# Optimization experiments

Hardware: AMD Instinct MI355X
Metric: run time of the kernel (lower is better)

## Reference

```python
import jax, jax.numpy as jnp
import numpy as np

B, S, E = 2, 2048, 2048
H, KV, D = 32, 8, 128
EPS = 1e-6


def _rope_tables(seq_len, head_dim, base=1_000_000.0):
    inv_freq = 1.0 / (base ** (np.arange(0, head_dim, 2, dtype=np.float32) / head_dim))
    ang = np.arange(seq_len, dtype=np.float32)[:, None] * inv_freq[None, :]  # [S, D/2]
    cos = np.concatenate([np.cos(ang), np.cos(ang)], axis=-1)  # [S, D]
    sin = np.concatenate([np.sin(ang), np.sin(ang)], axis=-1)
    return jnp.asarray(cos), jnp.asarray(sin)


def setup_inputs() -> dict:
    key = jax.random.key(0)
    ks = jax.random.split(key, 8)
    x = jax.random.normal(ks[0], (B, S, E), dtype=jnp.float32)
    mask = jnp.triu(jnp.ones((S, S), dtype=bool), k=1)  # True = masked (causal)
    cos, sin = _rope_tables(S, D)
    w = 0.02
    Wq = jax.random.normal(ks[1], (E, H * D), dtype=jnp.float32) * w
    bq = jnp.zeros((H * D,), dtype=jnp.float32)
    Wk = jax.random.normal(ks[2], (E, KV * D), dtype=jnp.float32) * w
    bk = jnp.zeros((KV * D,), dtype=jnp.float32)
    Wv = jax.random.normal(ks[3], (E, KV * D), dtype=jnp.float32) * w
    bv = jnp.zeros((KV * D,), dtype=jnp.float32)
    Wo = jax.random.normal(ks[4], (H * D, E), dtype=jnp.float32) * w
    q_scale = jnp.ones((D,), dtype=jnp.float32)
    k_scale = jnp.ones((D,), dtype=jnp.float32)
    return {"x": x, "mask": mask, "cos": cos, "sin": sin, "Wq": Wq, "bq": bq,
            "Wk": Wk, "bk": bk, "Wv": Wv, "bv": bv, "Wo": Wo,
            "q_scale": q_scale, "k_scale": k_scale}


def _rmsnorm(x, scale):
    xf = x.astype(jnp.float32)
    var = jnp.mean(xf * xf, axis=-1, keepdims=True)
    return (xf * jax.lax.rsqrt(var + EPS) * scale).astype(x.dtype)


def _apply_rope(x, cos, sin):
    # x: [B, h, S, D]; cos/sin: [S, D]
    d2 = x.shape[-1] // 2
    x1, x2 = x[..., :d2], x[..., d2:]
    rotated = jnp.concatenate([-x2, x1], axis=-1)
    return (x * cos[None, None] + rotated * sin[None, None]).astype(x.dtype)


def reference(x, mask, cos, sin, Wq, bq, Wk, bk, Wv, bv, Wo, q_scale, k_scale):
    b, s, _ = x.shape
    q = (x @ Wq + bq).reshape(b, s, H, D).transpose(0, 2, 1, 3)   # [B,H,S,D]
    k = (x @ Wk + bk).reshape(b, s, KV, D).transpose(0, 2, 1, 3)  # [B,KV,S,D]
    v = (x @ Wv + bv).reshape(b, s, KV, D).transpose(0, 2, 1, 3)
    q = _rmsnorm(q, q_scale)
    k = _rmsnorm(k, k_scale)
    q = _apply_rope(q, cos, sin)
    k = _apply_rope(k, cos, sin)
    group = H // KV
    k = jnp.repeat(k, group, axis=1)  # repeat_interleave on head dim -> [B,H,S,D]
    v = jnp.repeat(v, group, axis=1)
    scores = jnp.einsum("bhqd,bhkd->bhqk", q, k)
    scores = jnp.where(mask[None, None], -jnp.inf, scores)
    attn = jax.nn.softmax(scores / jnp.sqrt(jnp.float32(D)), axis=-1)
    ctx = jnp.einsum("bhqk,bhkd->bhqd", attn, v)
    ctx = ctx.transpose(0, 2, 1, 3).reshape(b, s, H * D)
    return ctx @ Wo
```

## Files before the change

### kernel.cpp

```cpp
#include <hip/hip_runtime.h>

typedef short short8 __attribute__((ext_vector_type(8)));
typedef float f32x4 __attribute__((ext_vector_type(4)));
typedef float f32x16 __attribute__((ext_vector_type(16)));
typedef unsigned int uint2v __attribute__((ext_vector_type(2)));

static __device__ __forceinline__ ushort f2bf(float f){
  union { float f; uint u; } cv; cv.f = f;
  uint u = cv.u;
  uint r = (u + 0x7fffu + ((u >> 16) & 1u)) >> 16;
  return (ushort)r;
}
static __device__ __forceinline__ float bf2f(ushort h){
  union { uint u; float f; } cv; cv.u = ((uint)h) << 16; return cv.f;
}
static __device__ __forceinline__ f32x4 mfma16x16x32(short8 a, short8 b, f32x4 c){
  return __builtin_amdgcn_mfma_f32_16x16x32_bf16(a, b, c, 0, 0, 0);
}
static __device__ __forceinline__ f32x16 mfma32(short8 a, short8 b, f32x16 c){
  return __builtin_amdgcn_mfma_f32_32x32x16_bf16(a, b, c, 0, 0, 0);
}
static __device__ __forceinline__ float ex2(float x){
  float r; asm("v_exp_f32 %0, %1" : "=v"(r) : "v"(x)); return r;
}
static __device__ __forceinline__ uint cvtpk(float lo, float hi){
  uint r; asm("v_cvt_pk_bf16_f32 %0, %1, %2" : "=v"(r) : "v"(lo), "v"(hi)); return r;
}
static __device__ __forceinline__ void glds16(const void* g, const void* l){
  __builtin_amdgcn_global_load_lds((const __attribute__((address_space(1))) void*)g,
                                   (__attribute__((address_space(3))) void*)l, 16, 0, 0);
}
static __device__ __forceinline__ void store_out(float* p, float v){ *p = v; }
static __device__ __forceinline__ void store_out(ushort* p, float v){ *p = f2bf(v); }
static __device__ __forceinline__ int xcd_swizzle(int flat, int nwg){
  int q = nwg >> 3, r = nwg & 7;
  int xcd = flat & 7, idx = flat >> 3;
  return (xcd < r) ? xcd * (q + 1) + idx : r * (q + 1) + (xcd - r) * q + idx;
}

__global__ void cvt_bf16_kernel(const float* __restrict__ x, ushort* __restrict__ y, int n4){
  int i = blockIdx.x * 256 + threadIdx.x;
  if (i < n4){
    float4 v = reinterpret_cast<const float4*>(x)[i];
    ushort4 o; o.x = f2bf(v.x); o.y = f2bf(v.y); o.z = f2bf(v.z); o.w = f2bf(v.w);
    reinterpret_cast<ushort4*>(y)[i] = o;
  }
}

__global__ void transpose_cvt_kernel(const float* __restrict__ W, ushort* __restrict__ WT, int K, int N){
  __shared__ float tile[32][33];
  int n0 = blockIdx.x * 32, k0 = blockIdx.y * 32;
  int tx = threadIdx.x, ty = threadIdx.y;
  #pragma unroll
  for (int i = 0; i < 4; i++){ int r = ty + i * 8; tile[r][tx] = W[(size_t)(k0 + r) * N + n0 + tx]; }
  __syncthreads();
  #pragma unroll
  for (int i = 0; i < 4; i++){ int r = ty + i * 8; WT[(size_t)(n0 + r) * K + k0 + tx] = f2bf(tile[tx][r]); }
}

__global__ void bias_concat_kernel(const float* __restrict__ bq, const float* __restrict__ bk,
                                   const float* __restrict__ bv, float* __restrict__ out){
  int i = blockIdx.x * 256 + threadIdx.x;
  if (i < 6144) out[i] = (i < 4096) ? bq[i] : ((i < 5120) ? bk[i - 4096] : bv[i - 5120]);
}

template<typename OutT>
__global__ __launch_bounds__(512, 2) void gemm256_kernel(const ushort* __restrict__ A, const ushort* __restrict__ BT,
                                                         const float* __restrict__ bias, OutT* __restrict__ C,
                                                         int M, int N, int K){
  __shared__ __align__(16) ushort As[2][128 * 64];
  __shared__ __align__(16) ushort Bs[2][256 * 64];
  const int nbx = N >> 8;
  const int nwg = nbx * (M >> 7);
  const int wg = xcd_swizzle(blockIdx.x, nwg);
  const int m0 = (wg / nbx) * 128, n0 = (wg % nbx) * 256;
  const int tid = threadIdx.x, w = tid >> 6, l = tid & 63, lm = l & 15, lk = l >> 4;
  const int wr = w >> 2, wc = w & 3;
  const int sr = tid >> 3, sc = tid & 7;
  const int scs = sc ^ (sr & 7);
  const int swz = lm & 7;
  const int nt = K >> 6;

#define STAGE_G(T, BUF) do{                                                                \
    _Pragma("unroll")                                                                      \
    for (int r = 0; r < 2; r++)                                                            \
      glds16(A + (size_t)(m0 + r * 64 + sr) * K + (size_t)(T) * 64 + scs * 8,              \
             &As[BUF][r * 4096 + w * 512]);                                                \
    _Pragma("unroll")                                                                      \
    for (int r = 0; r < 4; r++)                                                            \
      glds16(BT + (size_t)(n0 + r * 64 + sr) * K + (size_t)(T) * 64 + scs * 8,             \
             &Bs[BUF][r * 4096 + w * 512]);                                                \
  }while(0)

  f32x4 acc[4][4] = {};
  STAGE_G(0, 0);
  STAGE_G(1, 1);
  for (int t = 0; t < nt; t++){
    const int cur = t & 1;
    if (t < nt - 1) asm volatile("s_waitcnt vmcnt(6)" ::: "memory");
    else            asm volatile("s_waitcnt vmcnt(0)" ::: "memory");
    __builtin_amdgcn_s_barrier();
    asm volatile("" ::: "memory");
    short8 af[4][2], bf[4][2];
    #pragma unroll
    for (int mi = 0; mi < 4; mi++)
      #pragma unroll
      for (int ks = 0; ks < 2; ks++)
        af[mi][ks] = *(const short8*)&As[cur][(wr * 64 + mi * 16 + lm) * 64 + (((ks * 4 + lk) ^ swz) * 8)];
    #pragma unroll
    for (int ni = 0; ni < 4; ni++)
      #pragma unroll
      for (int ks = 0; ks < 2; ks++)
        bf[ni][ks] = *(const short8*)&Bs[cur][(wc * 64 + ni * 16 + lm) * 64 + (((ks * 4 + lk) ^ swz) * 8)];
    __builtin_amdgcn_s_setprio(1);
    #pragma unroll
    for (int mi = 0; mi < 4; mi++)
      #pragma unroll
      for (int ni = 0; ni < 4; ni++)
        #pragma unroll
        for (int ks = 0; ks < 2; ks++)
          acc[mi][ni] = mfma16x16x32(af[mi][ks], bf[ni][ks], acc[mi][ni]);
    __builtin_amdgcn_s_setprio(0);
    asm volatile("" ::: "memory");
    __builtin_amdgcn_s_barrier();
    if (t + 2 < nt) STAGE_G(t + 2, cur);
  }
#undef STAGE_G
  #pragma unroll
  for (int mi = 0; mi < 4; mi++)
    #pragma unroll
    for (int ni = 0; ni < 4; ni++){
      int col = n0 + wc * 64 + ni * 16 + lm;
      float bb = bias ? bias[col] : 0.0f;
      #pragma unroll
      for (int r = 0; r < 4; r++){
        int row = m0 + wr * 64 + mi * 16 + lk * 4 + r;
        store_out(&C[(size_t)row * N + col], acc[mi][ni][r] + bb);
      }
    }
}

#define QSCL2 0.12752016f
__global__ __launch_bounds__(256) void norm_rope_kernel(const ushort* __restrict__ qkv,
    const float* __restrict__ cosT, const float* __restrict__ sinT,
    const float* __restrict__ qs, const float* __restrict__ ksc,
    ushort* __restrict__ qo, ushort* __restrict__ ko, ushort* __restrict__ vto){
  int slot = blockIdx.x * 4 + (threadIdx.x >> 6);
  int lane = threadIdx.x & 63;
  int row = slot / 48, c = slot % 48;
  int b = row >> 11, s = row & 2047;
  size_t base = (size_t)row * 6144 + c * 128;
  float e1 = bf2f(qkv[base + lane]);
  float e2 = bf2f(qkv[base + lane + 64]);
  if (c < 40){
    float ss = e1 * e1 + e2 * e2;
    #pragma unroll
    for (int m = 1; m < 64; m <<= 1) ss += __shfl_xor(ss, m);
    float rs = rsqrtf(ss * (1.0f / 128.0f) + 1e-6f);
    const float* sc = (c < 32) ? qs : ksc;
    float n1 = e1 * rs * sc[lane], n2 = e2 * rs * sc[lane + 64];
    float c1 = cosT[s * 128 + lane],      s1 = sinT[s * 128 + lane];
    float c2 = cosT[s * 128 + lane + 64], s2 = sinT[s * 128 + lane + 64];
    float o1 = n1 * c1 - n2 * s1;
    float o2 = n2 * c2 + n1 * s2;
    if (c < 32){
      size_t ob = ((size_t)(b * 32 + c) * 2048 + s) * 128;
      qo[ob + lane] = f2bf(o1 * QSCL2); qo[ob + lane + 64] = f2bf(o2 * QSCL2);
    } else {
      int kv = c - 32;
      size_t ob = ((size_t)(b * 8 + kv) * 2048 + s) * 128;
      ko[ob + lane] = f2bf(o1); ko[ob + lane + 64] = f2bf(o2);
    }
  } else {
    int kv = c - 40;
    size_t ob = (size_t)(b * 8 + kv) * 128;
    vto[(ob + lane) * 2048 + s]      = f2bf(e1);
    vto[(ob + lane + 64) * 2048 + s] = f2bf(e2);
  }
}

__global__ __launch_bounds__(256, 2) void flash_kernel(const ushort* __restrict__ Q, const ushort* __restrict__ Kg,
    const ushort* __restrict__ VTg, ushort* __restrict__ ctx){
  __shared__ ushort Kl[2][64 * 128];
  __shared__ ushort Vl[2][128 * 64];
  const int bh = blockIdx.y, b = bh >> 5, h = bh & 31, kvh = h >> 2;
  const int bx = blockIdx.x;
  const int tid = threadIdx.x, w = tid >> 6, l = tid & 63;
  const int q31 = l & 31, hi = l >> 5, swz = q31 & 7;
  const ushort* Kbase = Kg  + (size_t)(b * 8 + kvh) * 2048 * 128;
  const ushort* Vbase = VTg + (size_t)(b * 8 + kvh) * 128 * 2048;
  const int krow = l >> 4, kcol = l & 15;
  const int vrow = l >> 3, vcol = l & 7;

  #define STAGE(KT, BS) do {                                                            \
    _Pragma("unroll")                                                                   \
    for (int i2 = 0; i2 < 4; i2++){                                                     \
      int i = w * 4 + i2; int row = i * 4 + krow;                                       \
      glds16(Kbase + (size_t)((KT) * 64 + row) * 128 + ((kcol ^ (row & 7)) * 8),        \
             &Kl[BS][i * 512]);                                                         \
    }                                                                                   \
    _Pragma("unroll")                                                                   \
    for (int j2 = 0; j2 < 4; j2++){                                                     \
      int j = w * 4 + j2; int row = j * 8 + vrow;                                       \
      glds16(Vbase + (size_t)row * 2048 + (KT) * 64 + ((vcol ^ (row & 7)) * 8),         \
             &Vl[BS][j * 512]);                                                         \
    }                                                                                   \
  } while (0)

  for (int pass = 0; pass < 2; pass++){
    const int qb = pass ? bx : (15 - bx);
    const int q0 = qb * 128;
    const int qw = q0 + w * 32;
    const int myq = qw + q31;
    const ushort* Qp = Q + ((size_t)(b * 32 + h) * 2048 + myq) * 128;
    short8 qf[8];
    #pragma unroll
    for (int s = 0; s < 8; s++) qf[s] = *(const short8*)(Qp + s * 16 + hi * 8);
    f32x16 o[4] = {};
    float m_r = -INFINITY, l_r = 0.f;
    const int nt = 2 * qb + 2;

    STAGE(0, 0);
    for (int kt = 0; kt < nt; kt++){
      const int cur = kt & 1;
      if (kt + 1 < nt){
        STAGE(kt + 1, cur ^ 1);
        asm volatile("s_waitcnt vmcnt(8)" ::: "memory");
      } else {
        asm volatile("s_waitcnt vmcnt(0)" ::: "memory");
      }
      __builtin_amdgcn_s_barrier();
      asm volatile("" ::: "memory");
      f32x16 sa0 = {}, sa1 = {};
      __builtin_amdgcn_s_setprio(1);
      #pragma unroll
      for (int s = 0; s < 8; s++){
        short8 a0 = *(const short8*)&Kl[cur][q31 * 128 + (((2 * s + hi) ^ swz) * 8)];
        short8 a1 = *(const short8*)&Kl[cur][(32 + q31) * 128 + (((2 * s + hi) ^ swz) * 8)];
        sa0 = mfma32(a0, qf[s], sa0);
        sa1 = mfma32(a1, qf[s], sa1);
      }
      __builtin_amdgcn_s_setprio(0);
      if (kt >= 2 * qb){
        #pragma unroll
        for (int r = 0; r < 16; r++){
          int krel = (r & 3) + 8 * (r >> 2) + 4 * hi;
          if (kt * 64 + krel > myq)      sa0[r] = -INFINITY;
          if (kt * 64 + 32 + krel > myq) sa1[r] = -INFINITY;
        }
      }
      float mx = fmaxf(sa0[0], sa1[0]);
      #pragma unroll
      for (int r = 1; r < 16; r++) mx = fmaxf(mx, fmaxf(sa0[r], sa1[r]));
      mx = fmaxf(mx, __shfl_xor(mx, 32));
      if (!__all(mx - m_r <= 8.f)){
        float mn = fmaxf(m_r, mx);
        float al = ex2(m_r - mn);
        m_r = mn; l_r *= al;
        #pragma unroll
        for (int r = 0; r < 16; r++){
          float alq = __shfl(al, (r & 3) + 8 * (r >> 2) + 4 * hi);
          o[0][r] *= alq; o[1][r] *= alq; o[2][r] *= alq; o[3][r] *= alq;
        }
      }
      float rsum = 0.f;
      #pragma unroll
      for (int r = 0; r < 16; r++){
        sa0[r] = ex2(sa0[r] - m_r);
        sa1[r] = ex2(sa1[r] - m_r);
        rsum += sa0[r] + sa1[r];
      }
      rsum += __shfl_xor(rsum, 32);
      l_r += rsum;
      uint pk0[8], pk1[8];
      #pragma unroll
      for (int t = 0; t < 8; t++){
        pk0[t] = cvtpk(sa0[2 * t], sa0[2 * t + 1]);
        pk1[t] = cvtpk(sa1[2 * t], sa1[2 * t + 1]);
      }
      __builtin_amdgcn_s_setprio(1);
      #pragma unroll
      for (int sub = 0; sub < 2; sub++){
        #pragma unroll
        for (int kc = 0; kc < 2; kc++){
          uint p0 = sub ? pk1[4 * kc]     : pk0[4 * kc];
          uint p1 = sub ? pk1[4 * kc + 1] : pk0[4 * kc + 1];
          uint p2 = sub ? pk1[4 * kc + 2] : pk0[4 * kc + 2];
          uint p3 = sub ? pk1[4 * kc + 3] : pk0[4 * kc + 3];
          uint2v r02 = __builtin_amdgcn_permlane32_swap(p0, p2, false, false);
          uint2v r13 = __builtin_amdgcn_permlane32_swap(p1, p3, false, false);
          union { uint u[4]; short8 v; } Af;
          Af.u[0] = r02[0]; Af.u[1] = r13[0]; Af.u[2] = r02[1]; Af.u[3] = r13[1];
          #pragma unroll
          for (int dc = 0; dc < 4; dc++){
            short8 vf = *(const short8*)&Vl[cur][(dc * 32 + q31) * 64 + (((4 * sub + 2 * kc + hi) ^ swz) * 8)];
            o[dc] = mfma32(Af.v, vf, o[dc]);
          }
        }
      }
      __builtin_amdgcn_s_setprio(0);
      asm volatile("" ::: "memory");
      __builtin_amdgcn_s_barrier();
    }
    float invl = 1.0f / l_r;
    ushort* Cp = ctx + (size_t)(b * 2048 + qw) * 4096 + (size_t)h * 128;
    #pragma unroll
    for (int r = 0; r < 16; r++){
      int qrel = (r & 3) + 8 * (r >> 2) + 4 * hi;
      float inv = __shfl(invl, qrel);
      #pragma unroll
      for (int dc = 0; dc < 4; dc++)
        Cp[(size_t)qrel * 4096 + dc * 32 + q31] = f2bf(o[dc][r] * inv);
    }
  }
  #undef STAGE
}

extern "C" void kernel_launch(void* const* d_in, const int* in_sizes, int n_in,
                              void* d_out, int out_size, void* d_ws, size_t ws_size,
                              hipStream_t stream){
  const float* x    = (const float*)d_in[0];
  const float* cosT = (const float*)d_in[2];
  const float* sinT = (const float*)d_in[3];
  const float* Wq   = (const float*)d_in[4];
  const float* bq   = (const float*)d_in[5];
  const float* Wk   = (const float*)d_in[6];
  const float* bk   = (const float*)d_in[7];
  const float* Wv   = (const float*)d_in[8];
  const float* bv   = (const float*)d_in[9];
  const float* Wo   = (const float*)d_in[10];
  const float* qs   = (const float*)d_in[11];
  const float* ksc  = (const float*)d_in[12];
  float* out = (float*)d_out;
  char* ws = (char*)d_ws;

  ushort* xb    = (ushort*)(ws + 0);
  ushort* wtqkv = (ushort*)(ws + 16777216);
  float*  biasq = (float* )(ws + 41943040);
  ushort* qkv   = (ushort*)(ws + 41967616);
  ushort* qb_   = (ushort*)(ws + 92299264);
  ushort* kb_   = (ushort*)(ws + 125853696);
  ushort* vtb   = (ushort*)(ws + 134242304);
  ushort* ctx   = (ushort*)(ws + 142630912);
  ushort* wot   = (ushort*)(ws + 176185344);

  cvt_bf16_kernel<<<8192, 256, 0, stream>>>(x, xb, 2097152);
  transpose_cvt_kernel<<<dim3(128, 64), dim3(32, 8), 0, stream>>>(Wq, wtqkv, 2048, 4096);
  transpose_cvt_kernel<<<dim3(32, 64),  dim3(32, 8), 0, stream>>>(Wk, wtqkv + (size_t)4096 * 2048, 2048, 1024);
  transpose_cvt_kernel<<<dim3(32, 64),  dim3(32, 8), 0, stream>>>(Wv, wtqkv + (size_t)5120 * 2048, 2048, 1024);
  transpose_cvt_kernel<<<dim3(64, 128), dim3(32, 8), 0, stream>>>(Wo, wot, 4096, 2048);
  bias_concat_kernel<<<24, 256, 0, stream>>>(bq, bk, bv, biasq);

  gemm256_kernel<ushort><<<768, 512, 0, stream>>>(xb, wtqkv, biasq, qkv, 4096, 6144, 2048);
  norm_rope_kernel<<<49152, 256, 0, stream>>>(qkv, cosT, sinT, qs, ksc, qb_, kb_, vtb);
  flash_kernel<<<dim3(8, 64), 256, 0, stream>>>(qb_, kb_, vtb, ctx);
  gemm256_kernel<float><<<256, 512, 0, stream>>>(ctx, wot, nullptr, out, 4096, 2048, 4096);
}
```

Measured before the change: 403.1 us.

## Use 256x256 GEMM tiles with interleaved LDS schedule and split-K output projection

The GEMM block tile grows from 128x256 to 256x256, and the main loop becomes a single-prefetch schedule. Global-to-LDS loads for the next tile are split into two halves and interleaved with quarter-block MFMA phases separated by barriers. The output projection now uses split-K (2 slices) writing fp32 partials into the reused qkv workspace, followed by an add kernel. This raises data reuse per block and keeps CUs busy for the smaller output GEMM. In exchange it doubles LDS (64KB->128KB per block) and accumulator registers, which likely lowers occupancy below the 2-block launch bound, and it adds a partial-sum round trip through memory.

```diff
diff --git a/kernel.cpp b/kernel.cpp
--- a/kernel.cpp
+++ b/kernel.cpp
@@ -44,6 +44,17 @@
     float4 v = reinterpret_cast<const float4*>(x)[i];
     ushort4 o; o.x = f2bf(v.x); o.y = f2bf(v.y); o.z = f2bf(v.z); o.w = f2bf(v.w);
     reinterpret_cast<ushort4*>(y)[i] = o;
+  }
+}
+
+__global__ void addk_kernel(const float* __restrict__ p0, const float* __restrict__ p1,
+                            float* __restrict__ out, int n4){
+  int i = blockIdx.x * 256 + threadIdx.x;
+  if (i < n4){
+    float4 a = reinterpret_cast<const float4*>(p0)[i];
+    float4 b = reinterpret_cast<const float4*>(p1)[i];
+    float4 o; o.x = a.x + b.x; o.y = a.y + b.y; o.z = a.z + b.z; o.w = a.w + b.w;
+    reinterpret_cast<float4*>(out)[i] = o;
   }
 }
 
@@ -67,75 +78,96 @@
 template<typename OutT>
 __global__ __launch_bounds__(512, 2) void gemm256_kernel(const ushort* __restrict__ A, const ushort* __restrict__ BT,
                                                          const float* __restrict__ bias, OutT* __restrict__ C,
-                                                         int M, int N, int K){
-  __shared__ __align__(16) ushort As[2][128 * 64];
+                                                         int M, int N, int K, int klen){
+  __shared__ __align__(16) ushort As[2][256 * 64];
   __shared__ __align__(16) ushort Bs[2][256 * 64];
   const int nbx = N >> 8;
-  const int nwg = nbx * (M >> 7);
+  const int nwg = nbx * (M >> 8);
   const int wg = xcd_swizzle(blockIdx.x, nwg);
-  const int m0 = (wg / nbx) * 128, n0 = (wg % nbx) * 256;
+  const int m0 = (wg / nbx) * 256, n0 = (wg % nbx) * 256;
+  const int kb = blockIdx.y * klen;
+  OutT* Cp = C + (size_t)blockIdx.y * M * N;
   const int tid = threadIdx.x, w = tid >> 6, l = tid & 63, lm = l & 15, lk = l >> 4;
   const int wr = w >> 2, wc = w & 3;
   const int sr = tid >> 3, sc = tid & 7;
   const int scs = sc ^ (sr & 7);
   const int swz = lm & 7;
-  const int nt = K >> 6;
-
-#define STAGE_G(T, BUF) do{                                                                \
-    _Pragma("unroll")                                                                      \
-    for (int r = 0; r < 2; r++)                                                            \
-      glds16(A + (size_t)(m0 + r * 64 + sr) * K + (size_t)(T) * 64 + scs * 8,              \
-             &As[BUF][r * 4096 + w * 512]);                                                \
-    _Pragma("unroll")                                                                      \
-    for (int r = 0; r < 4; r++)                                                            \
-      glds16(BT + (size_t)(n0 + r * 64 + sr) * K + (size_t)(T) * 64 + scs * 8,             \
-             &Bs[BUF][r * 4096 + w * 512]);                                                \
+  const int nt = klen >> 6;
+  const size_t abase = (size_t)(m0 + sr) * K + kb + scs * 8;
+  const size_t bbase = (size_t)(n0 + sr) * K + kb + scs * 8;
+
+#define STG_P(T, BUF, P) do{                                                                    \
+    glds16(A  + abase + (size_t)(2*(P))  *64*K + (T)*64, &As[BUF][(2*(P))  *4096 + w*512]);     \
+    glds16(A  + abase + (size_t)(2*(P)+1)*64*K + (T)*64, &As[BUF][(2*(P)+1)*4096 + w*512]);     \
+    glds16(BT + bbase + (size_t)(2*(P))  *64*K + (T)*64, &Bs[BUF][(2*(P))  *4096 + w*512]);     \
+    glds16(BT + bbase + (size_t)(2*(P)+1)*64*K + (T)*64, &Bs[BUF][(2*(P)+1)*4096 + w*512]);     \
   }while(0)
 
-  f32x4 acc[4][4] = {};
-  STAGE_G(0, 0);
-  STAGE_G(1, 1);
+#define RD_A(DST, RD, MB) do{                                                                   \
+    _Pragma("unroll")                                                                           \
+    for (int mi = 0; mi < 4; mi++)                                                              \
+      _Pragma("unroll")                                                                         \
+      for (int ks = 0; ks < 2; ks++)                                                            \
+        DST[mi][ks] = *(const short8*)&As[RD][(wr*128 + ((MB)+mi)*16 + lm)*64 + (((ks*4+lk)^swz)*8)]; \
+  }while(0)
+#define RD_B(DST, RD, NB) do{                                                                   \
+    _Pragma("unroll")                                                                           \
+    for (int ni = 0; ni < 2; ni++)                                                              \
+      _Pragma("unroll")                                                                         \
+      for (int ks = 0; ks < 2; ks++)                                                            \
+        DST[ni][ks] = *(const short8*)&Bs[RD][(wc*64 + ((NB)+ni)*16 + lm)*64 + (((ks*4+lk)^swz)*8)]; \
+  }while(0)
+#define MM(MB, NB, AF, BF) do{                                                                  \
+    __builtin_amdgcn_s_setprio(1);                                                             \
+    _Pragma("unroll")                                                                           \
+    for (int mi = 0; mi < 4; mi++)                                                              \
+      _Pragma("unroll")                                                                         \
+      for (int ni = 0; ni < 2; ni++)                                                            \
+        _Pragma("unroll")                                                                       \
+        for (int ks = 0; ks < 2; ks++)                                                          \
+          acc[(MB)+mi][(NB)+ni] = mfma16x16x32(AF[mi][ks], BF[ni][ks], acc[(MB)+mi][(NB)+ni]); \
+    __builtin_amdgcn_s_setprio(0);                                                             \
+  }while(0)
+
+  f32x4 acc[8][4] = {};
+  STG_P(0, 0, 0); STG_P(0, 0, 1);
   for (int t = 0; t < nt; t++){
-    const int cur = t & 1;
-    if (t < nt - 1) asm volatile("s_waitcnt vmcnt(6)" ::: "memory");
-    else            asm volatile("s_waitcnt vmcnt(0)" ::: "memory");
-    __builtin_amdgcn_s_barrier();
-    asm volatile("" ::: "memory");
-    short8 af[4][2], bf[4][2];
-    #pragma unroll
-    for (int mi = 0; mi < 4; mi++)
-      #pragma unroll
-      for (int ks = 0; ks < 2; ks++)
-        af[mi][ks] = *(const short8*)&As[cur][(wr * 64 + mi * 16 + lm) * 64 + (((ks * 4 + lk) ^ swz) * 8)];
-    #pragma unroll
-    for (int ni = 0; ni < 4; ni++)
-      #pragma unroll
-      for (int ks = 0; ks < 2; ks++)
-        bf[ni][ks] = *(const short8*)&Bs[cur][(wc * 64 + ni * 16 + lm) * 64 + (((ks * 4 + lk) ^ swz) * 8)];
-    __builtin_amdgcn_s_setprio(1);
-    #pragma unroll
-    for (int mi = 0; mi < 4; mi++)
-      #pragma unroll
-      for (int ni = 0; ni < 4; ni++)
-        #pragma unroll
-        for (int ks = 0; ks < 2; ks++)
-          acc[mi][ni] = mfma16x16x32(af[mi][ks], bf[ni][ks], acc[mi][ni]);
-    __builtin_amdgcn_s_setprio(0);
-    asm volatile("" ::: "memory");
-    __builtin_amdgcn_s_barrier();
-    if (t + 2 < nt) STAGE_G(t + 2, cur);
-  }
-#undef STAGE_G
+    const int rd = t & 1, wb = rd ^ 1;
+    const bool pf = (t + 1 < nt);
+    if (pf) STG_P(t + 1, wb, 0);
+    if (pf) asm volatile("s_waitcnt vmcnt(4)" ::: "memory");
+    else    asm volatile("s_waitcnt vmcnt(0)" ::: "memory");
+    __builtin_amdgcn_s_barrier();
+    short8 af[4][2], bf01[2][2], bf23[2][2];
+    RD_A(af, rd, 0); RD_B(bf01, rd, 0);
+    __builtin_amdgcn_s_barrier();
+    MM(0, 0, af, bf01);
+    __builtin_amdgcn_s_barrier();
+    RD_B(bf23, rd, 2);
+    if (pf) STG_P(t + 1, wb, 1);
+    __builtin_amdgcn_s_barrier();
+    MM(0, 2, af, bf23);
+    __builtin_amdgcn_s_barrier();
+    RD_A(af, rd, 4);
+    __builtin_amdgcn_s_barrier();
+    MM(4, 2, af, bf23);
+    __builtin_amdgcn_s_barrier();
+    MM(4, 0, af, bf01);
+  }
+#undef STG_P
+#undef RD_A
+#undef RD_B
+#undef MM
   #pragma unroll
-  for (int mi = 0; mi < 4; mi++)
+  for (int mi = 0; mi < 8; mi++)
     #pragma unroll
     for (int ni = 0; ni < 4; ni++){
       int col = n0 + wc * 64 + ni * 16 + lm;
       float bb = bias ? bias[col] : 0.0f;
       #pragma unroll
       for (int r = 0; r < 4; r++){
-        int row = m0 + wr * 64 + mi * 16 + lk * 4 + r;
-        store_out(&C[(size_t)row * N + col], acc[mi][ni][r] + bb);
+        int row = m0 + wr * 128 + mi * 16 + lk * 4 + r;
+        store_out(&Cp[(size_t)row * N + col], acc[mi][ni][r] + bb);
       }
     }
 }
@@ -343,6 +375,7 @@
   ushort* vtb   = (ushort*)(ws + 134242304);
   ushort* ctx   = (ushort*)(ws + 142630912);
   ushort* wot   = (ushort*)(ws + 176185344);
+  float* part   = (float*)(ws + 41967616);
 
   cvt_bf16_kernel<<<8192, 256, 0, stream>>>(x, xb, 2097152);
   transpose_cvt_kernel<<<dim3(128, 64), dim3(32, 8), 0, stream>>>(Wq, wtqkv, 2048, 4096);
@@ -351,8 +384,9 @@
   transpose_cvt_kernel<<<dim3(64, 128), dim3(32, 8), 0, stream>>>(Wo, wot, 4096, 2048);
   bias_concat_kernel<<<24, 256, 0, stream>>>(bq, bk, bv, biasq);
 
-  gemm256_kernel<ushort><<<768, 512, 0, stream>>>(xb, wtqkv, biasq, qkv, 4096, 6144, 2048);
+  gemm256_kernel<ushort><<<dim3(384, 1), 512, 0, stream>>>(xb, wtqkv, biasq, qkv, 4096, 6144, 2048, 2048);
   norm_rope_kernel<<<49152, 256, 0, stream>>>(qkv, cosT, sinT, qs, ksc, qb_, kb_, vtb);
   flash_kernel<<<dim3(8, 64), 256, 0, stream>>>(qb_, kb_, vtb, ctx);
-  gemm256_kernel<float><<<256, 512, 0, stream>>>(ctx, wot, nullptr, out, 4096, 2048, 4096);
-}
+  gemm256_kernel<float><<<dim3(128, 2), 512, 0, stream>>>(ctx, wot, nullptr, part, 4096, 2048, 4096, 2048);
+  addk_kernel<<<8192, 256, 0, stream>>>(part, part + (size_t)4096 * 2048, out, 2097152);
+}
```

Result: slower. 418.5 us (+3.8%).

## Template GEMM with BK=32 double buffering and smaller tiles for output projection

Applied to the files above, without the earlier changes.

Replaces the fixed 128x256 GEMM, which used a K-step of 64 and prefetched two steps ahead, with a templated double-buffered kernel. The new kernel uses a K-step of 32 and issues the next tile's loads just before computing the current one. The LDS footprint per block is halved, and launch bounds now scale with the wave count. The output projection moves to a 128x128 tile with 256 threads, giving 512 blocks instead of 256 so more CUs are busy. The cost is twice as many barriers per K and less prefetch depth, which may expose more memory latency.

```diff
diff --git a/kernel.cpp b/kernel.cpp
--- a/kernel.cpp
+++ b/kernel.cpp
@@ -64,77 +64,78 @@
   if (i < 6144) out[i] = (i < 4096) ? bq[i] : ((i < 5120) ? bk[i - 4096] : bv[i - 5120]);
 }
 
-template<typename OutT>
-__global__ __launch_bounds__(512, 2) void gemm256_kernel(const ushort* __restrict__ A, const ushort* __restrict__ BT,
-                                                         const float* __restrict__ bias, OutT* __restrict__ C,
-                                                         int M, int N, int K){
-  __shared__ __align__(16) ushort As[2][128 * 64];
-  __shared__ __align__(16) ushort Bs[2][256 * 64];
-  const int nbx = N >> 8;
-  const int nwg = nbx * (M >> 7);
+template<typename OutT, int WR, int WC, int MR, int NR>
+__global__ __launch_bounds__(WR*WC*64, (WR*WC*64)/128)
+void gemm_db_kernel(const ushort* __restrict__ A, const ushort* __restrict__ BT,
+                    const float* __restrict__ bias, OutT* __restrict__ C,
+                    int M, int N, int K){
+  constexpr int NWV = WR * WC, T = NWV * 64;
+  constexpr int BM = WR * MR * 16, BN = WC * NR * 16;
+  constexpr int RA = BM * 4 / T, RB = BN * 4 / T;
+  constexpr int L = RA + RB;
+  __shared__ __align__(16) ushort As[2][BM * 32];
+  __shared__ __align__(16) ushort Bs[2][BN * 32];
+  const int nbx = N / BN;
+  const int nwg = nbx * (M / BM);
   const int wg = xcd_swizzle(blockIdx.x, nwg);
-  const int m0 = (wg / nbx) * 128, n0 = (wg % nbx) * 256;
+  const int m0 = (wg / nbx) * BM, n0 = (wg % nbx) * BN;
   const int tid = threadIdx.x, w = tid >> 6, l = tid & 63, lm = l & 15, lk = l >> 4;
-  const int wr = w >> 2, wc = w & 3;
-  const int sr = tid >> 3, sc = tid & 7;
-  const int scs = sc ^ (sr & 7);
-  const int swz = lm & 7;
-  const int nt = K >> 6;
-
-#define STAGE_G(T, BUF) do{                                                                \
+  const int wr = w / WC, wc = w % WC;
+  const int rchunk = lk ^ (lm & 3);
+  const int nt = K >> 5;
+
+#define STAGE_T(TK, BUF) do{                                                               \
     _Pragma("unroll")                                                                      \
-    for (int r = 0; r < 2; r++)                                                            \
-      glds16(A + (size_t)(m0 + r * 64 + sr) * K + (size_t)(T) * 64 + scs * 8,              \
-             &As[BUF][r * 4096 + w * 512]);                                                \
+    for (int r = 0; r < RA; r++){                                                          \
+      int s = r * T + tid, row = s >> 2, ch = (s & 3) ^ (row & 3);                         \
+      glds16(A + (size_t)(m0 + row) * K + (TK) * 32 + ch * 8, &As[BUF][s * 8]);            \
+    }                                                                                      \
     _Pragma("unroll")                                                                      \
-    for (int r = 0; r < 4; r++)                                                            \
-      glds16(BT + (size_t)(n0 + r * 64 + sr) * K + (size_t)(T) * 64 + scs * 8,             \
-             &Bs[BUF][r * 4096 + w * 512]);                                                \
+    for (int r = 0; r < RB; r++){                                                          \
+      int s = r * T + tid, row = s >> 2, ch = (s & 3) ^ (row & 3);                         \
+      glds16(BT + (size_t)(n0 + row) * K + (TK) * 32 + ch * 8, &Bs[BUF][s * 8]);           \
+    }                                                                                      \
   }while(0)
 
-  f32x4 acc[4][4] = {};
-  STAGE_G(0, 0);
-  STAGE_G(1, 1);
+  f32x4 acc[MR][NR] = {};
+  STAGE_T(0, 0);
   for (int t = 0; t < nt; t++){
     const int cur = t & 1;
-    if (t < nt - 1) asm volatile("s_waitcnt vmcnt(6)" ::: "memory");
-    else            asm volatile("s_waitcnt vmcnt(0)" ::: "memory");
+    if (t + 1 < nt){
+      STAGE_T(t + 1, cur ^ 1);
+      if constexpr (L == 3) asm volatile("s_waitcnt vmcnt(3)" ::: "memory");
+      else if constexpr (L == 4) asm volatile("s_waitcnt vmcnt(4)" ::: "memory");
+      else asm volatile("s_waitcnt vmcnt(0)" ::: "memory");
+    } else {
+      asm volatile("s_waitcnt vmcnt(0)" ::: "memory");
+    }
     __builtin_amdgcn_s_barrier();
-    asm volatile("" ::: "memory");
-    short8 af[4][2], bf[4][2];
-    #pragma unroll
-    for (int mi = 0; mi < 4; mi++)
-      #pragma unroll
-      for (int ks = 0; ks < 2; ks++)
-        af[mi][ks] = *(const short8*)&As[cur][(wr * 64 + mi * 16 + lm) * 64 + (((ks * 4 + lk) ^ swz) * 8)];
-    #pragma unroll
-    for (int ni = 0; ni < 4; ni++)
-      #pragma unroll
-      for (int ks = 0; ks < 2; ks++)
-        bf[ni][ks] = *(const short8*)&Bs[cur][(wc * 64 + ni * 16 + lm) * 64 + (((ks * 4 + lk) ^ swz) * 8)];
+    short8 af[MR], bf[NR];
+    #pragma unroll
+    for (int mi = 0; mi < MR; mi++)
+      af[mi] = *(const short8*)&As[cur][(wr * MR * 16 + mi * 16 + lm) * 32 + rchunk * 8];
+    #pragma unroll
+    for (int ni = 0; ni < NR; ni++)
+      bf[ni] = *(const short8*)&Bs[cur][(wc * NR * 16 + ni * 16 + lm) * 32 + rchunk * 8];
     __builtin_amdgcn_s_setprio(1);
     #pragma unroll
-    for (int mi = 0; mi < 4; mi++)
-      #pragma unroll
-      for (int ni = 0; ni < 4; ni++)
-        #pragma unroll
-        for (int ks = 0; ks < 2; ks++)
-          acc[mi][ni] = mfma16x16x32(af[mi][ks], bf[ni][ks], acc[mi][ni]);
+    for (int mi = 0; mi < MR; mi++)
+      #pragma unroll
+      for (int ni = 0; ni < NR; ni++)
+        acc[mi][ni] = mfma16x16x32(af[mi], bf[ni], acc[mi][ni]);
     __builtin_amdgcn_s_setprio(0);
-    asm volatile("" ::: "memory");
     __builtin_amdgcn_s_barrier();
-    if (t + 2 < nt) STAGE_G(t + 2, cur);
   }
-#undef STAGE_G
+#undef STAGE_T
   #pragma unroll
-  for (int mi = 0; mi < 4; mi++)
-    #pragma unroll
-    for (int ni = 0; ni < 4; ni++){
-      int col = n0 + wc * 64 + ni * 16 + lm;
+  for (int mi = 0; mi < MR; mi++)
+    #pragma unroll
+    for (int ni = 0; ni < NR; ni++){
+      int col = n0 + wc * NR * 16 + ni * 16 + lm;
       float bb = bias ? bias[col] : 0.0f;
       #pragma unroll
       for (int r = 0; r < 4; r++){
-        int row = m0 + wr * 64 + mi * 16 + lk * 4 + r;
+        int row = m0 + wr * MR * 16 + mi * 16 + lk * 4 + r;
         store_out(&C[(size_t)row * N + col], acc[mi][ni][r] + bb);
       }
     }
@@ -351,8 +352,8 @@
   transpose_cvt_kernel<<<dim3(64, 128), dim3(32, 8), 0, stream>>>(Wo, wot, 4096, 2048);
   bias_concat_kernel<<<24, 256, 0, stream>>>(bq, bk, bv, biasq);
 
-  gemm256_kernel<ushort><<<768, 512, 0, stream>>>(xb, wtqkv, biasq, qkv, 4096, 6144, 2048);
+  gemm_db_kernel<ushort, 2, 4, 4, 4><<<768, 512, 0, stream>>>(xb, wtqkv, biasq, qkv, 4096, 6144, 2048);
   norm_rope_kernel<<<49152, 256, 0, stream>>>(qkv, cosT, sinT, qs, ksc, qb_, kb_, vtb);
   flash_kernel<<<dim3(8, 64), 256, 0, stream>>>(qb_, kb_, vtb, ctx);
-  gemm256_kernel<float><<<256, 512, 0, stream>>>(ctx, wot, nullptr, out, 4096, 2048, 4096);
-}
+  gemm_db_kernel<float, 2, 2, 4, 4><<<512, 256, 0, stream>>>(ctx, wot, nullptr, out, 4096, 2048, 4096);
+}
```

Result: no change. 405.3 us (+0.5%).

## Shrink GEMM tile to 128x128 with 256 threads and restructure prefetch

Applied to the files above, without the earlier changes.

Replaces the 128x256 tile, 512-thread GEMM with a 128x128 tile, 256-thread kernel, doubling the workgroup count for both projection GEMMs. The prefetch schedule changes from issuing two stages ahead after compute to issuing the next stage at the top of each iteration, before waiting on the current one. More workgroups should fill the 256 CUs better and use less LDS per workgroup. In exchange each K-tile of data is reused less and more global traffic is spent per FLOP.

```diff
diff --git a/kernel.cpp b/kernel.cpp
--- a/kernel.cpp
+++ b/kernel.cpp
@@ -14,7 +14,7 @@
 static __device__ __forceinline__ float bf2f(ushort h){
   union { uint u; float f; } cv; cv.u = ((uint)h) << 16; return cv.f;
 }
-static __device__ __forceinline__ f32x4 mfma16x16x32(short8 a, short8 b, f32x4 c){
+static __device__ __forceinline__ f32x4 mfma16(short8 a, short8 b, f32x4 c){
   return __builtin_amdgcn_mfma_f32_16x16x32_bf16(a, b, c, 0, 0, 0);
 }
 static __device__ __forceinline__ f32x16 mfma32(short8 a, short8 b, f32x16 c){
@@ -65,40 +65,43 @@
 }
 
 template<typename OutT>
-__global__ __launch_bounds__(512, 2) void gemm256_kernel(const ushort* __restrict__ A, const ushort* __restrict__ BT,
-                                                         const float* __restrict__ bias, OutT* __restrict__ C,
-                                                         int M, int N, int K){
+__global__ __launch_bounds__(256, 2)
+void gemm_c2_kernel(const ushort* __restrict__ A, const ushort* __restrict__ BT,
+                    const float* __restrict__ bias, OutT* __restrict__ C,
+                    int M, int N, int K){
   __shared__ __align__(16) ushort As[2][128 * 64];
-  __shared__ __align__(16) ushort Bs[2][256 * 64];
-  const int nbx = N >> 8;
+  __shared__ __align__(16) ushort Bs[2][128 * 64];
+  const int nbx = N >> 7;
   const int nwg = nbx * (M >> 7);
   const int wg = xcd_swizzle(blockIdx.x, nwg);
-  const int m0 = (wg / nbx) * 128, n0 = (wg % nbx) * 256;
+  const int m0 = (wg / nbx) * 128, n0 = (wg % nbx) * 128;
   const int tid = threadIdx.x, w = tid >> 6, l = tid & 63, lm = l & 15, lk = l >> 4;
-  const int wr = w >> 2, wc = w & 3;
-  const int sr = tid >> 3, sc = tid & 7;
-  const int scs = sc ^ (sr & 7);
-  const int swz = lm & 7;
+  const int wr = w >> 1, wc = w & 1;
   const int nt = K >> 6;
 
-#define STAGE_G(T, BUF) do{                                                                \
+#define STAGE_T(TK, BUF) do{                                                               \
     _Pragma("unroll")                                                                      \
-    for (int r = 0; r < 2; r++)                                                            \
-      glds16(A + (size_t)(m0 + r * 64 + sr) * K + (size_t)(T) * 64 + scs * 8,              \
-             &As[BUF][r * 4096 + w * 512]);                                                \
+    for (int r = 0; r < 4; r++){                                                           \
+      int s = r * 256 + tid, row = s >> 3, ch = (s & 7) ^ (row & 7);                       \
+      glds16(A + (size_t)(m0 + row) * K + (size_t)(TK) * 64 + ch * 8, &As[BUF][s * 8]);    \
+    }                                                                                      \
     _Pragma("unroll")                                                                      \
-    for (int r = 0; r < 4; r++)                                                            \
-      glds16(BT + (size_t)(n0 + r * 64 + sr) * K + (size_t)(T) * 64 + scs * 8,             \
-             &Bs[BUF][r * 4096 + w * 512]);                                                \
+    for (int r = 0; r < 4; r++){                                                           \
+      int s = r * 256 + tid, row = s >> 3, ch = (s & 7) ^ (row & 7);                       \
+      glds16(BT + (size_t)(n0 + row) * K + (size_t)(TK) * 64 + ch * 8, &Bs[BUF][s * 8]);   \
+    }                                                                                      \
   }while(0)
 
   f32x4 acc[4][4] = {};
-  STAGE_G(0, 0);
-  STAGE_G(1, 1);
+  STAGE_T(0, 0);
   for (int t = 0; t < nt; t++){
     const int cur = t & 1;
-    if (t < nt - 1) asm volatile("s_waitcnt vmcnt(6)" ::: "memory");
-    else            asm volatile("s_waitcnt vmcnt(0)" ::: "memory");
+    if (t + 1 < nt){
+      STAGE_T(t + 1, cur ^ 1);
+      asm volatile("s_waitcnt vmcnt(8)" ::: "memory");
+    } else {
+      asm volatile("s_waitcnt vmcnt(0)" ::: "memory");
+    }
     __builtin_amdgcn_s_barrier();
     asm volatile("" ::: "memory");
     short8 af[4][2], bf[4][2];
@@ -106,12 +109,12 @@
     for (int mi = 0; mi < 4; mi++)
       #pragma unroll
       for (int ks = 0; ks < 2; ks++)
-        af[mi][ks] = *(const short8*)&As[cur][(wr * 64 + mi * 16 + lm) * 64 + (((ks * 4 + lk) ^ swz) * 8)];
+        af[mi][ks] = *(const short8*)&As[cur][(wr * 64 + mi * 16 + lm) * 64 + (((ks * 4 + lk) ^ (lm & 7)) * 8)];
     #pragma unroll
     for (int ni = 0; ni < 4; ni++)
       #pragma unroll
       for (int ks = 0; ks < 2; ks++)
-        bf[ni][ks] = *(const short8*)&Bs[cur][(wc * 64 + ni * 16 + lm) * 64 + (((ks * 4 + lk) ^ swz) * 8)];
+        bf[ni][ks] = *(const short8*)&Bs[cur][(wc * 64 + ni * 16 + lm) * 64 + (((ks * 4 + lk) ^ (lm & 7)) * 8)];
     __builtin_amdgcn_s_setprio(1);
     #pragma unroll
     for (int mi = 0; mi < 4; mi++)
@@ -119,13 +122,12 @@
       for (int ni = 0; ni < 4; ni++)
         #pragma unroll
         for (int ks = 0; ks < 2; ks++)
-          acc[mi][ni] = mfma16x16x32(af[mi][ks], bf[ni][ks], acc[mi][ni]);
+          acc[mi][ni] = mfma16(af[mi][ks], bf[ni][ks], acc[mi][ni]);
     __builtin_amdgcn_s_setprio(0);
     asm volatile("" ::: "memory");
     __builtin_amdgcn_s_barrier();
-    if (t + 2 < nt) STAGE_G(t + 2, cur);
   }
-#undef STAGE_G
+#undef STAGE_T
   #pragma unroll
   for (int mi = 0; mi < 4; mi++)
     #pragma unroll
@@ -351,8 +353,8 @@
   transpose_cvt_kernel<<<dim3(64, 128), dim3(32, 8), 0, stream>>>(Wo, wot, 4096, 2048);
   bias_concat_kernel<<<24, 256, 0, stream>>>(bq, bk, bv, biasq);
 
-  gemm256_kernel<ushort><<<768, 512, 0, stream>>>(xb, wtqkv, biasq, qkv, 4096, 6144, 2048);
+  gemm_c2_kernel<ushort><<<1536, 256, 0, stream>>>(xb, wtqkv, biasq, qkv, 4096, 6144, 2048);
   norm_rope_kernel<<<49152, 256, 0, stream>>>(qkv, cosT, sinT, qs, ksc, qb_, kb_, vtb);
   flash_kernel<<<dim3(8, 64), 256, 0, stream>>>(qb_, kb_, vtb, ctx);
-  gemm256_kernel<float><<<256, 512, 0, stream>>>(ctx, wot, nullptr, out, 4096, 2048, 4096);
-}
+  gemm_c2_kernel<float><<<512, 256, 0, stream>>>(ctx, wot, nullptr, out, 4096, 2048, 4096);
+}
```

Result: faster. 384.4 us (median of 2 runs) (-4.6%).
